# Optimization experiments

Hardware: AMD Instinct MI355X
Metric: run time of the kernel (lower is better)

The kernel has to match this reference:

```python
import jax, jax.numpy as jnp
import numpy as np

FDIM = 512
NUM_HEADS = 8
FATT = FDIM // NUM_HEADS  # 64


def setup_inputs() -> dict:
    key = jax.random.key(0)
    ks = jax.random.split(key, 8)
    Nx, Np = 2048, 4096
    s = 0.05
    return {
        "fx_in": jax.random.normal(ks[0], (Nx, FDIM), jnp.float32),
        "fp_in": jax.random.normal(ks[1], (1, Np, FDIM), jnp.float32),
        "Wembd": jax.random.normal(ks[2], (NUM_HEADS, FATT, FDIM), jnp.float32) * s,
        "bembd": jax.random.normal(ks[3], (NUM_HEADS, FATT), jnp.float32) * s,
        "Wfc": jax.random.normal(ks[4], (NUM_HEADS, FATT, 2 * FATT), jnp.float32) * s,
        "bfc": jax.random.normal(ks[5], (NUM_HEADS, FATT), jnp.float32) * s,
        "Wout": jax.random.normal(ks[6], (FDIM, FATT * NUM_HEADS), jnp.float32) * s,
        "bout": jax.random.normal(ks[7], (FDIM,), jnp.float32) * s,
    }


def reference(fx_in, fp_in, Wembd, bembd, Wfc, bfc, Wout, bout):
    # fx_in: [Nx, F]; fp_in: [1, Np, F] -> squeeze leading dim
    fp0 = fp_in[0]
    Nx = fx_in.shape[0]
    d = jnp.sqrt(jnp.asarray(FATT, fx_in.dtype))
    # per-head embedding of concatenated [fx; fp]: [H, Nx+Np, e]
    f = jnp.concatenate([fx_in, fp0], axis=0)
    femb = jnp.einsum('nf,hef->hne', f, Wembd) + bembd[:, None, :]
    fx, fp = femb[:, :Nx], femb[:, Nx:]          # [H,Nx,e], [H,Np,e]
    # attention weights (dropout is identity in eval)
    scores = jnp.einsum('hxe,hpe->hxp', fx, fp) / d
    w = jax.nn.softmax(scores, axis=2)            # [H,Nx,Np]
    # gather + concat + per-head fuse MLP
    fa_att = jnp.einsum('hxp,hpe->hxe', w, fp)    # [H,Nx,e]
    fa = jnp.concatenate([fa_att, fx], axis=2)    # [H,Nx,2e]
    fa = jax.nn.relu(jnp.einsum('hxc,hec->hxe', fa, Wfc) + bfc[:, None, :])
    fa = jnp.transpose(fa, (1, 0, 2)).reshape(Nx, -1)  # [Nx, H*e]
    fx_out = jax.nn.relu(fx_in + fa @ Wout.T + bout)
    w_out = jnp.transpose(w, (1, 0, 2))           # [Nx, H, Np]
    return fx_out, w_out
```

## Files before the change

kernel.cpp:

```cpp
#include <hip/hip_runtime.h>

typedef unsigned short ushort_t;
using frag_ab = __attribute__((ext_vector_type(8))) short;
using f32x4   = __attribute__((ext_vector_type(4))) float;
using u32x4   = __attribute__((ext_vector_type(4))) unsigned int;
using u32x2   = __attribute__((ext_vector_type(2))) unsigned int;

#define FDIM 512
#define NH 8
#define FATT 64
#define NX 2048
#define NP 4096
#define NTOT 6144

__device__ __forceinline__ ushort_t f2bf(float f) {
    unsigned u = __float_as_uint(f);
    u = (u + 0x7FFFu + ((u >> 16) & 1u)) >> 16;
    return (ushort_t)u;
}
__device__ __forceinline__ float bf2f(ushort_t s) {
    return __uint_as_float(((unsigned)s) << 16);
}
__device__ __forceinline__ unsigned pk2bf(float a, float b) {
    return (unsigned)f2bf(a) | ((unsigned)f2bf(b) << 16);
}

__global__ __launch_bounds__(256) void k_prep(const float* __restrict__ fx,
                                              const float* __restrict__ fp,
                                              const float* __restrict__ We,
                                              const float* __restrict__ Wfc,
                                              const float* __restrict__ Wout,
                                              ushort_t* __restrict__ f_b,
                                              ushort_t* __restrict__ We_b,
                                              ushort_t* __restrict__ Wfc_b,
                                              ushort_t* __restrict__ Wout_b) {
    int i = blockIdx.x * 256 + threadIdx.x;
    int stride = gridDim.x * 256;
    const int NF4 = NTOT * FDIM / 4;
    const int NX4 = NX * FDIM / 4;
    for (int idx = i; idx < NF4; idx += stride) {
        float4 v = (idx < NX4) ? ((const float4*)fx)[idx]
                               : ((const float4*)fp)[idx - NX4];
        ushort4 o;
        o.x = f2bf(v.x); o.y = f2bf(v.y); o.z = f2bf(v.z); o.w = f2bf(v.w);
        ((ushort4*)f_b)[idx] = o;
    }
    const int NW4 = FDIM * FDIM / 4;
    for (int idx = i; idx < NW4; idx += stride) {
        float4 v = ((const float4*)We)[idx];
        ushort4 o;
        o.x = f2bf(v.x); o.y = f2bf(v.y); o.z = f2bf(v.z); o.w = f2bf(v.w);
        ((ushort4*)We_b)[idx] = o;
    }
    const int NFC4 = NH * FATT * 2 * FATT / 4;
    for (int idx = i; idx < NFC4; idx += stride) {
        float4 v = ((const float4*)Wfc)[idx];
        ushort4 o;
        o.x = f2bf(v.x); o.y = f2bf(v.y); o.z = f2bf(v.z); o.w = f2bf(v.w);
        ((ushort4*)Wfc_b)[idx] = o;
    }
    for (int idx = i; idx < NW4; idx += stride) {
        float4 v = ((const float4*)Wout)[idx];
        ushort4 o;
        o.x = f2bf(v.x); o.y = f2bf(v.y); o.z = f2bf(v.z); o.w = f2bf(v.w);
        ((ushort4*)Wout_b)[idx] = o;
    }
}

__global__ __launch_bounds__(256) void k_embed(const ushort_t* __restrict__ f_b,
                                               const ushort_t* __restrict__ We_b,
                                               const float* __restrict__ bembd,
                                               ushort_t* __restrict__ femb_b,
                                               ushort_t* __restrict__ fpT_b,
                                               ushort_t* __restrict__ facat_b) {
    int tid = threadIdx.x;
    int wv = tid >> 6, lane = tid & 63;
    int g = lane >> 4, c = lane & 15;
    int m0 = blockIdx.x * 64 + wv * 16;
    int o0 = blockIdx.y * 64;

    f32x4 acc[4] = {};
    const ushort_t* arow = f_b + (size_t)(m0 + c) * FDIM + g * 8;
#pragma unroll 4
    for (int ks = 0; ks < FDIM; ks += 32) {
        frag_ab a = *(const frag_ab*)(arow + ks);
#pragma unroll
        for (int t = 0; t < 4; ++t) {
            const ushort_t* brow = We_b + (size_t)(o0 + t * 16 + c) * FDIM + ks + g * 8;
            frag_ab b = *(const frag_ab*)brow;
            acc[t] = __builtin_amdgcn_mfma_f32_16x16x32_bf16(a, b, acc[t], 0, 0, 0);
        }
    }
#pragma unroll
    for (int t = 0; t < 4; ++t) {
        int o = o0 + t * 16 + c;
        int h = o >> 6, e = o & 63;
        float bia = bembd[o];
#pragma unroll
        for (int r = 0; r < 4; ++r) {
            int n = m0 + g * 4 + r;
            ushort_t v = f2bf(acc[t][r] + bia);
            femb_b[((size_t)h * NTOT + n) * FATT + e] = v;
            if (n >= NX) fpT_b[((size_t)h * FATT + e) * NP + (n - NX)] = v;
            else         facat_b[((size_t)h * NX + n) * 128 + 64 + e] = v;
        }
    }
}

__global__ __launch_bounds__(1024) void k_attn_p1(const ushort_t* __restrict__ femb_b,
                                                  const ushort_t* __restrict__ fpT_b,
                                                  float* __restrict__ inv_sums,
                                                  ushort_t* __restrict__ facat_b) {
    int bid = blockIdx.x;
    int h  = bid & 7;
    int xb = bid >> 3;
    int tid = threadIdx.x;
    int wv = tid >> 6;
    int lane = tid & 63;
    int g = lane >> 4, c = lane & 15;

    __shared__ float lds_pv[64][68];
    __shared__ float lds_sum[64];
    __shared__ float lds_inv[64];

    const ushort_t* fxb = femb_b + (size_t)h * NTOT * FATT;
    const ushort_t* fpb = fxb + (size_t)NX * FATT;
    const ushort_t* fTb = fpT_b + (size_t)h * FATT * NP;

    frag_ab bx0_0, bx0_1, bx1_0, bx1_1, bx2_0, bx2_1, bx3_0, bx3_1;
    {
        const ushort_t* b0 = fxb + (size_t)(xb * 64 + 0 * 16 + c) * FATT + g * 8;
        const ushort_t* b1 = fxb + (size_t)(xb * 64 + 1 * 16 + c) * FATT + g * 8;
        const ushort_t* b2 = fxb + (size_t)(xb * 64 + 2 * 16 + c) * FATT + g * 8;
        const ushort_t* b3 = fxb + (size_t)(xb * 64 + 3 * 16 + c) * FATT + g * 8;
        bx0_0 = *(const frag_ab*)b0;  bx0_1 = *(const frag_ab*)(b0 + 32);
        bx1_0 = *(const frag_ab*)b1;  bx1_1 = *(const frag_ab*)(b1 + 32);
        bx2_0 = *(const frag_ab*)b2;  bx2_1 = *(const frag_ab*)(b2 + 32);
        bx3_0 = *(const frag_ab*)b3;  bx3_1 = *(const frag_ab*)(b3 + 32);
    }

    f32x4 pacc[4][4] = {};
    float rsum[4] = {0.f, 0.f, 0.f, 0.f};
    const int p0 = wv * 256;

    for (int ps = p0; ps < p0 + 256; ps += 16) {
        const ushort_t* ar = fpb + (size_t)(ps + c) * FATT + g * 8;
        frag_ab a0 = *(const frag_ab*)ar;
        frag_ab a1 = *(const frag_ab*)(ar + 32);
        frag_ab pb[4];
#pragma unroll
        for (int xg = 0; xg < 4; ++xg) {
            frag_ab q0 = (xg == 0) ? bx0_0 : (xg == 1) ? bx1_0 : (xg == 2) ? bx2_0 : bx3_0;
            frag_ab q1 = (xg == 0) ? bx0_1 : (xg == 1) ? bx1_1 : (xg == 2) ? bx2_1 : bx3_1;
            f32x4 s = {};
            s = __builtin_amdgcn_mfma_f32_16x16x32_bf16(a0, q0, s, 0, 0, 0);
            s = __builtin_amdgcn_mfma_f32_16x16x32_bf16(a1, q1, s, 0, 0, 0);
            float e0 = __expf(s[0] * 0.125f);
            float e1 = __expf(s[1] * 0.125f);
            float e2 = __expf(s[2] * 0.125f);
            float e3 = __expf(s[3] * 0.125f);
            rsum[xg] += (e0 + e1) + (e2 + e3);
            u32x4 bw;
            bw[0] = pk2bf(e0, e1);
            bw[1] = pk2bf(e2, e3);
            bw[2] = 0u;
            bw[3] = 0u;
            pb[xg] = __builtin_bit_cast(frag_ab, bw);
        }
#pragma unroll
        for (int t2 = 0; t2 < 4; ++t2) {
            const ushort_t* vr = fTb + (size_t)(t2 * 16 + c) * NP + ps + g * 4;
            u32x2 vl = *(const u32x2*)vr;
            u32x4 aw;
            aw[0] = vl[0];
            aw[1] = vl[1];
            aw[2] = 0u;
            aw[3] = 0u;
            frag_ab va = __builtin_bit_cast(frag_ab, aw);
#pragma unroll
            for (int xg = 0; xg < 4; ++xg)
                pacc[xg][t2] = __builtin_amdgcn_mfma_f32_16x16x32_bf16(va, pb[xg], pacc[xg][t2], 0, 0, 0);
        }
    }

#pragma unroll
    for (int xg = 0; xg < 4; ++xg) {
        rsum[xg] += __shfl_xor(rsum[xg], 16);
        rsum[xg] += __shfl_xor(rsum[xg], 32);
    }

    for (int w = 0; w < 16; ++w) {
        if (wv == w) {
            if (w == 0) {
                if (lane < 16) {
#pragma unroll
                    for (int xg = 0; xg < 4; ++xg) lds_sum[xg * 16 + c] = rsum[xg];
                }
#pragma unroll
                for (int xg = 0; xg < 4; ++xg)
#pragma unroll
                    for (int t2 = 0; t2 < 4; ++t2)
                        *(f32x4*)&lds_pv[xg * 16 + c][t2 * 16 + 4 * g] = pacc[xg][t2];
            } else {
                if (lane < 16) {
#pragma unroll
                    for (int xg = 0; xg < 4; ++xg) lds_sum[xg * 16 + c] += rsum[xg];
                }
#pragma unroll
                for (int xg = 0; xg < 4; ++xg)
#pragma unroll
                    for (int t2 = 0; t2 < 4; ++t2) {
                        f32x4 cur = *(const f32x4*)&lds_pv[xg * 16 + c][t2 * 16 + 4 * g];
                        cur += pacc[xg][t2];
                        *(f32x4*)&lds_pv[xg * 16 + c][t2 * 16 + 4 * g] = cur;
                    }
            }
        }
        __syncthreads();
    }
    if (tid < 64) {
        float inv = 1.f / lds_sum[tid];
        lds_inv[tid] = inv;
        inv_sums[(size_t)h * NX + xb * 64 + tid] = inv;
    }
    __syncthreads();

    if (tid < 512) {
        int row = tid >> 3;
        int e0 = (tid & 7) * 8;
        float inv = lds_inv[row];
        u32x4 o;
#pragma unroll
        for (int j = 0; j < 4; ++j)
            o[j] = pk2bf(lds_pv[row][e0 + 2 * j] * inv, lds_pv[row][e0 + 2 * j + 1] * inv);
        *(u32x4*)&facat_b[((size_t)h * NX + xb * 64 + row) * 128 + e0] = o;
    }
}

__global__ __launch_bounds__(256) void k_wout(const ushort_t* __restrict__ femb_b,
                                              const float* __restrict__ inv_sums,
                                              float* __restrict__ w_out) {
    int bid = blockIdx.x;
    int h    = bid & 7;
    int rest = bid >> 3;
    int xb   = rest & 31;
    int sl   = rest >> 5;
    int tid = threadIdx.x;
    int wv = tid >> 6;
    int lane = tid & 63;
    int g = lane >> 4, c = lane & 15;

    __shared__ float lds[4][16][132];

    const ushort_t* fxb = femb_b + (size_t)h * NTOT * FATT;
    const ushort_t* fpb = fxb + (size_t)NX * FATT;

    frag_ab q0[4], q1[4];
    float inv[4];
#pragma unroll
    for (int xg = 0; xg < 4; ++xg) {
        const ushort_t* b = fxb + (size_t)(xb * 64 + xg * 16 + c) * FATT + g * 8;
        q0[xg] = *(const frag_ab*)b;
        q1[xg] = *(const frag_ab*)(b + 32);
        inv[xg] = inv_sums[(size_t)h * NX + xb * 64 + xg * 16 + c];
    }

    const int p_base = sl * 1024 + wv * 256;
    for (int chunk = 0; chunk < 2; ++chunk) {
        int pc = p_base + chunk * 128;
        frag_ab af0[8], af1[8];
#pragma unroll
        for (int pt = 0; pt < 8; ++pt) {
            const ushort_t* ar = fpb + (size_t)(pc + pt * 16 + c) * FATT + g * 8;
            af0[pt] = *(const frag_ab*)ar;
            af1[pt] = *(const frag_ab*)(ar + 32);
        }
#pragma unroll
        for (int xg = 0; xg < 4; ++xg) {
#pragma unroll
            for (int pt = 0; pt < 8; ++pt) {
                f32x4 s = {};
                s = __builtin_amdgcn_mfma_f32_16x16x32_bf16(af0[pt], q0[xg], s, 0, 0, 0);
                s = __builtin_amdgcn_mfma_f32_16x16x32_bf16(af1[pt], q1[xg], s, 0, 0, 0);
                f32x4 ev;
                ev[0] = __expf(s[0] * 0.125f) * inv[xg];
                ev[1] = __expf(s[1] * 0.125f) * inv[xg];
                ev[2] = __expf(s[2] * 0.125f) * inv[xg];
                ev[3] = __expf(s[3] * 0.125f) * inv[xg];
                int sw = (pt * 16 + g * 4) ^ ((c & 7) << 4);
                *(f32x4*)&lds[wv][c][sw] = ev;
            }
#pragma unroll
            for (int row = 0; row < 16; ++row) {
                int pi = lane * 2;
                int swr = pi ^ ((row & 7) << 4);
                float2 v = *(const float2*)&lds[wv][row][swr];
                float* dst = w_out + ((size_t)(xb * 64 + xg * 16 + row) * NH + h) * NP + pc + pi;
                *(float2*)dst = v;
            }
        }
    }
}

__global__ __launch_bounds__(256) void k_fc(const ushort_t* __restrict__ facat_b,
                                            const ushort_t* __restrict__ Wfc_b,
                                            const float* __restrict__ bfc,
                                            ushort_t* __restrict__ fcout_b) {
    int tid = threadIdx.x;
    int wv = tid >> 6, lane = tid & 63;
    int g = lane >> 4, c = lane & 15;
    int x0 = blockIdx.x * 64 + wv * 16;
    int h = blockIdx.y;

    const ushort_t* A = facat_b + ((size_t)h * NX + x0 + c) * 128 + g * 8;
    const ushort_t* B = Wfc_b + (size_t)h * FATT * 128;

    f32x4 acc[4] = {};
#pragma unroll
    for (int ks = 0; ks < 128; ks += 32) {
        frag_ab a = *(const frag_ab*)(A + ks);
#pragma unroll
        for (int t = 0; t < 4; ++t) {
            frag_ab b = *(const frag_ab*)(B + (size_t)(t * 16 + c) * 128 + ks + g * 8);
            acc[t] = __builtin_amdgcn_mfma_f32_16x16x32_bf16(a, b, acc[t], 0, 0, 0);
        }
    }
#pragma unroll
    for (int t = 0; t < 4; ++t) {
        int e = t * 16 + c;
        float bia = bfc[h * FATT + e];
#pragma unroll
        for (int r = 0; r < 4; ++r) {
            int x = x0 + g * 4 + r;
            fcout_b[(size_t)x * FDIM + h * FATT + e] = f2bf(fmaxf(acc[t][r] + bia, 0.f));
        }
    }
}

__global__ __launch_bounds__(256) void k_out(const float* __restrict__ fx_in,
                                             const ushort_t* __restrict__ fcout_b,
                                             const ushort_t* __restrict__ Wout_b,
                                             const float* __restrict__ bout,
                                             float* __restrict__ out) {
    int tid = threadIdx.x;
    int wv = tid >> 6, lane = tid & 63;
    int g = lane >> 4, c = lane & 15;
    int x0 = blockIdx.x * 64 + wv * 16;
    int o0 = blockIdx.y * 64;

    f32x4 acc[4] = {};
    const ushort_t* A = fcout_b + (size_t)(x0 + c) * FDIM + g * 8;
#pragma unroll 4
    for (int ks = 0; ks < FDIM; ks += 32) {
        frag_ab a = *(const frag_ab*)(A + ks);
#pragma unroll
        for (int t = 0; t < 4; ++t) {
            frag_ab b = *(const frag_ab*)(Wout_b + (size_t)(o0 + t * 16 + c) * FDIM + ks + g * 8);
            acc[t] = __builtin_amdgcn_mfma_f32_16x16x32_bf16(a, b, acc[t], 0, 0, 0);
        }
    }
#pragma unroll
    for (int t = 0; t < 4; ++t) {
        int f = o0 + t * 16 + c;
        float bia = bout[f];
#pragma unroll
        for (int r = 0; r < 4; ++r) {
            int x = x0 + g * 4 + r;
            float v = acc[t][r] + bia + fx_in[(size_t)x * FDIM + f];
            out[(size_t)x * FDIM + f] = fmaxf(v, 0.f);
        }
    }
}

extern "C" void kernel_launch(void* const* d_in, const int* in_sizes, int n_in,
                              void* d_out, int out_size, void* d_ws, size_t ws_size,
                              hipStream_t stream) {
    const float* fx_in = (const float*)d_in[0];
    const float* fp_in = (const float*)d_in[1];
    const float* Wembd = (const float*)d_in[2];
    const float* bembd = (const float*)d_in[3];
    const float* Wfc   = (const float*)d_in[4];
    const float* bfc   = (const float*)d_in[5];
    const float* Wout  = (const float*)d_in[6];
    const float* bout  = (const float*)d_in[7];

    float* out   = (float*)d_out;
    float* w_out = out + (size_t)NX * FDIM;

    ushort_t* f_b     = (ushort_t*)d_ws;
    ushort_t* We_b    = f_b + (size_t)NTOT * FDIM;
    ushort_t* femb_b  = We_b + (size_t)FDIM * FDIM;
    ushort_t* fpT_b   = femb_b + (size_t)NH * NTOT * FATT;
    ushort_t* facat_b = fpT_b + (size_t)NH * FATT * NP;
    ushort_t* fcout_b = facat_b + (size_t)NH * NX * 128;
    ushort_t* Wfc_b   = fcout_b + (size_t)NX * FDIM;
    ushort_t* Wout_b  = Wfc_b + (size_t)NH * FATT * 2 * FATT;
    float*    inv_sums= (float*)(Wout_b + (size_t)FDIM * FDIM);

    k_prep   <<<1024, 256, 0, stream>>>(fx_in, fp_in, Wembd, Wfc, Wout,
                                        f_b, We_b, Wfc_b, Wout_b);
    k_embed  <<<dim3(96, 8), 256, 0, stream>>>(f_b, We_b, bembd, femb_b, fpT_b, facat_b);
    k_attn_p1<<<256, 1024, 0, stream>>>(femb_b, fpT_b, inv_sums, facat_b);
    k_wout   <<<1024, 256, 0, stream>>>(femb_b, inv_sums, w_out);
    k_fc     <<<dim3(32, 8), 256, 0, stream>>>(facat_b, Wfc_b, bfc, fcout_b);
    k_out    <<<dim3(32, 8), 256, 0, stream>>>(fx_in, fcout_b, Wout_b, bout, out);
}
```

Before: 197.7 us.

## Write attention weights directly from registers and halve attn_p1 block size

The w_out kernel no longer stages scores through a swizzled LDS tile for coalesced float2 row stores. It writes each MFMA output fragment straight to global memory as float4 stores, and uses twice as many blocks, each covering 512 p positions. The attention-sum kernel moves from 1024 to 512 threads per block, with each wave covering 512 p positions, so the cross-wave LDS reduction has 8 serial steps instead of 16. The direct stores are less coalesced, with 16-byte pieces scattered across 16 rows, which risks poorer write efficiency on the large 268MB w_out output.

Result: faster. 179.2 us (-9.3%).

```diff
diff --git a/kernel.cpp b/kernel.cpp
--- a/kernel.cpp
+++ b/kernel.cpp
@@ -107,10 +107,10 @@
     }
 }
 
-__global__ __launch_bounds__(1024) void k_attn_p1(const ushort_t* __restrict__ femb_b,
-                                                  const ushort_t* __restrict__ fpT_b,
-                                                  float* __restrict__ inv_sums,
-                                                  ushort_t* __restrict__ facat_b) {
+__global__ __launch_bounds__(512) void k_attn_p1(const ushort_t* __restrict__ femb_b,
+                                                 const ushort_t* __restrict__ fpT_b,
+                                                 float* __restrict__ inv_sums,
+                                                 ushort_t* __restrict__ facat_b) {
     int bid = blockIdx.x;
     int h  = bid & 7;
     int xb = bid >> 3;
@@ -141,9 +141,9 @@
 
     f32x4 pacc[4][4] = {};
     float rsum[4] = {0.f, 0.f, 0.f, 0.f};
-    const int p0 = wv * 256;
-
-    for (int ps = p0; ps < p0 + 256; ps += 16) {
+    const int p0 = wv * 512;
+
+    for (int ps = p0; ps < p0 + 512; ps += 16) {
         const ushort_t* ar = fpb + (size_t)(ps + c) * FATT + g * 8;
         frag_ab a0 = *(const frag_ab*)ar;
         frag_ab a1 = *(const frag_ab*)(ar + 32);
@@ -189,7 +189,7 @@
         rsum[xg] += __shfl_xor(rsum[xg], 32);
     }
 
-    for (int w = 0; w < 16; ++w) {
+    for (int w = 0; w < 8; ++w) {
         if (wv == w) {
             if (w == 0) {
                 if (lane < 16) {
@@ -225,7 +225,7 @@
     }
     __syncthreads();
 
-    if (tid < 512) {
+    {
         int row = tid >> 3;
         int e0 = (tid & 7) * 8;
         float inv = lds_inv[row];
@@ -250,8 +250,6 @@
     int lane = tid & 63;
     int g = lane >> 4, c = lane & 15;
 
-    __shared__ float lds[4][16][132];
-
     const ushort_t* fxb = femb_b + (size_t)h * NTOT * FATT;
     const ushort_t* fpb = fxb + (size_t)NX * FATT;
 
@@ -265,39 +263,23 @@
         inv[xg] = inv_sums[(size_t)h * NX + xb * 64 + xg * 16 + c];
     }
 
-    const int p_base = sl * 1024 + wv * 256;
-    for (int chunk = 0; chunk < 2; ++chunk) {
-        int pc = p_base + chunk * 128;
-        frag_ab af0[8], af1[8];
-#pragma unroll
-        for (int pt = 0; pt < 8; ++pt) {
-            const ushort_t* ar = fpb + (size_t)(pc + pt * 16 + c) * FATT + g * 8;
-            af0[pt] = *(const frag_ab*)ar;
-            af1[pt] = *(const frag_ab*)(ar + 32);
-        }
+    const int p0 = sl * 512 + wv * 128;
+    for (int ps = p0; ps < p0 + 128; ps += 16) {
+        const ushort_t* ar = fpb + (size_t)(ps + c) * FATT + g * 8;
+        frag_ab a0 = *(const frag_ab*)ar;
+        frag_ab a1 = *(const frag_ab*)(ar + 32);
 #pragma unroll
         for (int xg = 0; xg < 4; ++xg) {
-#pragma unroll
-            for (int pt = 0; pt < 8; ++pt) {
-                f32x4 s = {};
-                s = __builtin_amdgcn_mfma_f32_16x16x32_bf16(af0[pt], q0[xg], s, 0, 0, 0);
-                s = __builtin_amdgcn_mfma_f32_16x16x32_bf16(af1[pt], q1[xg], s, 0, 0, 0);
-                f32x4 ev;
-                ev[0] = __expf(s[0] * 0.125f) * inv[xg];
-                ev[1] = __expf(s[1] * 0.125f) * inv[xg];
-                ev[2] = __expf(s[2] * 0.125f) * inv[xg];
-                ev[3] = __expf(s[3] * 0.125f) * inv[xg];
-                int sw = (pt * 16 + g * 4) ^ ((c & 7) << 4);
-                *(f32x4*)&lds[wv][c][sw] = ev;
-            }
-#pragma unroll
-            for (int row = 0; row < 16; ++row) {
-                int pi = lane * 2;
-                int swr = pi ^ ((row & 7) << 4);
-                float2 v = *(const float2*)&lds[wv][row][swr];
-                float* dst = w_out + ((size_t)(xb * 64 + xg * 16 + row) * NH + h) * NP + pc + pi;
-                *(float2*)dst = v;
-            }
+            f32x4 s = {};
+            s = __builtin_amdgcn_mfma_f32_16x16x32_bf16(a0, q0[xg], s, 0, 0, 0);
+            s = __builtin_amdgcn_mfma_f32_16x16x32_bf16(a1, q1[xg], s, 0, 0, 0);
+            f32x4 o;
+            o[0] = __expf(s[0] * 0.125f) * inv[xg];
+            o[1] = __expf(s[1] * 0.125f) * inv[xg];
+            o[2] = __expf(s[2] * 0.125f) * inv[xg];
+            o[3] = __expf(s[3] * 0.125f) * inv[xg];
+            float* dst = w_out + ((size_t)(xb * 64 + xg * 16 + c) * NH + h) * NP + ps + g * 4;
+            *(f32x4*)dst = o;
         }
     }
 }
@@ -400,8 +382,8 @@
     k_prep   <<<1024, 256, 0, stream>>>(fx_in, fp_in, Wembd, Wfc, Wout,
                                         f_b, We_b, Wfc_b, Wout_b);
     k_embed  <<<dim3(96, 8), 256, 0, stream>>>(f_b, We_b, bembd, femb_b, fpT_b, facat_b);
-    k_attn_p1<<<256, 1024, 0, stream>>>(femb_b, fpT_b, inv_sums, facat_b);
-    k_wout   <<<1024, 256, 0, stream>>>(femb_b, inv_sums, w_out);
+    k_attn_p1<<<256, 512, 0, stream>>>(femb_b, fpT_b, inv_sums, facat_b);
+    k_wout   <<<2048, 256, 0, stream>>>(femb_b, inv_sums, w_out);
     k_fc     <<<dim3(32, 8), 256, 0, stream>>>(facat_b, Wfc_b, bfc, fcout_b);
     k_out    <<<dim3(32, 8), 256, 0, stream>>>(fx_in, fcout_b, Wout_b, bout, out);
 }
```
